# Kernel optimization log

Measured on AMD Instinct MI355X. Metric: run time of the kernel, lower is better.

## Reference

```python
import jax, jax.numpy as jnp
import numpy as np

RADIUS_IN, RADIUS_OUT, NSAMPLE = 0.4, 0.8, 32
SCENE = 10.0  # cube edge length for point coordinates


def setup_inputs() -> dict:
    key = jax.random.key(0)
    k1, k2, k3 = jax.random.split(key, 3)
    B, N, NP, C = 2, 16384, 4096, 64
    xyz = jax.random.uniform(k1, (B, N, 3), dtype=jnp.float32) * SCENE
    new_xyz = jax.random.uniform(k2, (B, NP, 3), dtype=jnp.float32) * SCENE
    features = jax.random.normal(k3, (B, C, N), dtype=jnp.float32)
    return {"xyz": xyz, "new_xyz": new_xyz, "features": features}


def ball_query_dilated(xyz, new_xyz, min_r, max_r, nsample):
    # xyz: (B,N,3), new_xyz: (B,P,3) -> idx: (B,P,nsample) int32
    N = xyz.shape[1]
    d2 = jnp.sum((new_xyz[:, :, None, :] - xyz[:, None, :, :]) ** 2, axis=-1)  # (B,P,N)
    mask = (d2 >= min_r * min_r) & (d2 < max_r * max_r)
    ar = jnp.arange(N, dtype=jnp.int32)
    # valid points keep their index; invalid pushed after all valid ones, in order
    sort_key = jnp.where(mask, ar, ar + N)
    _, idx_sorted = jax.lax.top_k(-sort_key, nsample)  # first nsample in-range point indices
    cnt = jnp.sum(mask, axis=-1)  # (B,P)
    slot_valid = jnp.arange(nsample, dtype=cnt.dtype)[None, None, :] < cnt[:, :, None]
    # CUDA kernel fills all slots with the first found index; if none found idx stays 0
    # (when cnt==0, idx_sorted[...,0] == 0 since key N is the minimum), so this matches.
    idx = jnp.where(slot_valid, idx_sorted, idx_sorted[:, :, :1])
    return idx.astype(jnp.int32)


def group(features, idx):
    # features: (B,C,N), idx: (B,P,S) -> (B,C,P,S)
    return jax.vmap(lambda f, i: f[:, i])(features, idx)


def reference(xyz, new_xyz, features):
    idx = ball_query_dilated(xyz, new_xyz, RADIUS_IN, RADIUS_OUT, NSAMPLE)
    xyz_t = jnp.transpose(xyz, (0, 2, 1))  # (B,3,N)
    grouped_xyz = group(xyz_t, idx) - jnp.transpose(new_xyz, (0, 2, 1))[:, :, :, None]
    grouped_features = group(features, idx)
    new_features = jnp.concatenate([grouped_xyz, grouped_features], axis=1)  # (B,3+C,P,S)
    return new_features
```

## Files before the change

### kernel.cpp

```cpp
#include <hip/hip_runtime.h>
#include <hip/hip_bf16.h>

#define BB 2
#define NN 16384
#define NP 4096
#define CC 64
#define SS 32
#define NCH (3 + CC)

#define NSUB 32
#define SUBN (NN / NSUB)

__global__ void __launch_bounds__(256) pack_xyz_kernel(
    const float* __restrict__ xyz, float4* __restrict__ xyz4)
{
    int i = blockIdx.x * 256 + threadIdx.x;
    if (i < BB * NN) {
        float4 v;
        v.x = xyz[3 * i + 0];
        v.y = xyz[3 * i + 1];
        v.z = xyz[3 * i + 2];
        v.w = 0.0f;
        xyz4[i] = v;
    }
}

__global__ void __launch_bounds__(256) transpose_feat_kernel(
    const float* __restrict__ f, float* __restrict__ ft)
{
    __shared__ float tile[64 * 65];
    const int b  = blockIdx.y;
    const int n0 = blockIdx.x * 64;
    const int t  = threadIdx.x;
    const int tn  = t & 63;
    const int tc4 = t >> 6;
#pragma unroll
    for (int r = 0; r < 16; ++r) {
        int c = r * 4 + tc4;
        tile[c * 65 + tn] = f[((b * CC + c) << 14) + n0 + tn];
    }
    __syncthreads();
#pragma unroll
    for (int r = 0; r < 16; ++r) {
        int nl = r * 4 + tc4;
        ft[((b << 14) + n0 + nl) * CC + tn] = tile[tn * 65 + nl];
    }
}

__global__ void __launch_bounds__(256) query_kernel(
    const float4* __restrict__ xyz4, const float* __restrict__ new_xyz,
    unsigned short* __restrict__ part, unsigned char* __restrict__ cntp)
{
#pragma clang fp contract(off)
    __shared__ float4 pts_s[SUBN];
    const int t   = threadIdx.x;
    const int sub = blockIdx.y;
    const int q   = blockIdx.x * 256 + t;
    const int b   = q >> 12;

    const float RMIN2 = (float)(0.4 * 0.4);
    const float RMAX2 = (float)(0.8 * 0.8);
    const unsigned ULO = __float_as_uint(RMIN2);
    const unsigned URNG = __float_as_uint(RMAX2) - ULO;

    const float4* __restrict__ pts = xyz4 + (b << 14) + sub * SUBN;
#pragma unroll
    for (int i = 0; i < SUBN / 256; ++i)
        pts_s[i * 256 + t] = pts[i * 256 + t];
    __syncthreads();

    const float qx = new_xyz[q * 3 + 0];
    const float qy = new_xyz[q * 3 + 1];
    const float qz = new_xyz[q * 3 + 2];

    unsigned short* __restrict__ mypart = part + (q * NSUB + sub) * SS;
    const int base = sub * SUBN;

    int cnt = 0;
    for (int j0 = 0; j0 < SUBN; j0 += 8) {
        float4 P[8];
#pragma unroll
        for (int k = 0; k < 8; ++k) P[k] = pts_s[j0 + k];
        unsigned m = 0;
#pragma unroll
        for (int k = 0; k < 8; ++k) {
            float dx = P[k].x - qx;
            float dy = P[k].y - qy;
            float dz = P[k].z - qz;
            float dx2 = dx * dx;
            float dy2 = dy * dy;
            float dz2 = dz * dz;
            float d2 = (dx2 + dy2) + dz2;
            unsigned ud = __float_as_uint(d2);
            bool valid = (ud - ULO) < URNG;
            m |= valid ? (1u << k) : 0u;
        }
        if (m) {
            do {
                int k = __ffs(m) - 1;
                m &= m - 1;
                if (cnt < SS) {
                    mypart[cnt] = (unsigned short)(base + j0 + k);
                    cnt++;
                }
            } while (m);
        }
    }
    cntp[q * NSUB + sub] = (unsigned char)cnt;
}

__global__ void __launch_bounds__(256) merge_kernel(
    const unsigned short* __restrict__ part, const unsigned char* __restrict__ cntp,
    int* __restrict__ idxg)
{
    const int lane = threadIdx.x & 63;
    const int w    = threadIdx.x >> 6;
    const int q    = blockIdx.x * 4 + w;

    int c = (lane < NSUB) ? (int)cntp[q * NSUB + lane] : 0;

    int off = c;
#pragma unroll
    for (int d = 1; d < 64; d <<= 1) {
        int v = __shfl_up(off, d);
        if (lane >= d) off += v;
    }
    int total = __shfl(off, 63);
    if (total > SS) total = SS;
    off -= c;

    const unsigned short* __restrict__ p = part + (q * NSUB + lane) * SS;
    int firstval = (c > 0) ? (int)p[0] : 0;
    unsigned long long m = __ballot(c > 0);
    int first = 0;
    if (m) {
        int fl = __ffsll((unsigned long long)m) - 1;
        first = __shfl(firstval, fl);
    }

    int* __restrict__ o = idxg + q * SS;
    for (int j = 0; j < c; ++j) {
        int s = off + j;
        if (s < SS) o[s] = (int)p[j];
    }
    if (lane < SS && lane >= total) o[lane] = first;
}

__global__ void __launch_bounds__(256) group_kernel(
    const float4* __restrict__ xyz4, const float* __restrict__ new_xyz,
    const float* __restrict__ ft, const int* __restrict__ idxg,
    float* __restrict__ out)
{
    __shared__ float tile[4][16 * 66];
    const int w    = threadIdx.x >> 6;
    const int lane = threadIdx.x & 63;
    const int q    = blockIdx.x * 4 + w;
    const int b    = q >> 12;
    const int p    = q & (NP - 1);
    const int s    = lane & 31;

    const int idxv = idxg[q * SS + s];

    float4 pt = xyz4[(b << 14) + idxv];
    float q0 = new_xyz[q * 3 + 0];
    float q1 = new_xyz[q * 3 + 1];
    float q2 = new_xyz[q * 3 + 2];
    if (lane < 32) {
        out[((b * NCH + 0) * NP + p) * SS + s] = pt.x - q0;
        out[((b * NCH + 1) * NP + p) * SS + s] = pt.y - q1;
        out[((b * NCH + 2) * NP + p) * SS + s] = pt.z - q2;
    }

    float* tl = tile[w];
    const float* __restrict__ ftb = ft + (b << 14) * CC;
    const int sl = lane & 15;
    const int cq = lane >> 4;
#pragma unroll
    for (int h = 0; h < 2; ++h) {
#pragma unroll
        for (int s2 = 0; s2 < 16; ++s2) {
            int n = __shfl(idxv, h * 16 + s2);
            tl[s2 * 66 + lane] = ftb[(n << 6) + lane];
        }
        asm volatile("s_waitcnt lgkmcnt(0)" ::: "memory");
#pragma unroll
        for (int cp = 0; cp < 16; ++cp) {
            int ch = cp * 4 + cq;
            out[((b * NCH + 3 + ch) * NP + p) * SS + h * 16 + sl] = tl[sl * 66 + ch];
        }
        asm volatile("s_waitcnt lgkmcnt(0)" ::: "memory");
    }
}

extern "C" void kernel_launch(void* const* d_in, const int* in_sizes, int n_in,
                              void* d_out, int out_size, void* d_ws, size_t ws_size,
                              hipStream_t stream)
{
    const float* xyz      = (const float*)d_in[0];
    const float* new_xyz  = (const float*)d_in[1];
    const float* features = (const float*)d_in[2];
    float* out = (float*)d_out;

    char* ws = (char*)d_ws;
    float4*         xyz4 = (float4*)(ws);
    float*          ft   = (float*)(ws + 524288);
    unsigned short* part = (unsigned short*)(ws + 8912896);
    unsigned char*  cntp = (unsigned char*)(ws + 25690112);
    int*            idxg = (int*)(ws + 25952256);

    hipLaunchKernelGGL(pack_xyz_kernel, dim3((BB * NN) / 256), dim3(256), 0, stream,
                       xyz, xyz4);
    hipLaunchKernelGGL(transpose_feat_kernel, dim3(NN / 64, BB), dim3(256), 0, stream,
                       features, ft);
    hipLaunchKernelGGL(query_kernel, dim3((BB * NP) / 256, NSUB), dim3(256), 0, stream,
                       xyz4, new_xyz, part, cntp);
    hipLaunchKernelGGL(merge_kernel, dim3((BB * NP) / 4), dim3(256), 0, stream,
                       part, cntp, idxg);
    hipLaunchKernelGGL(group_kernel, dim3((BB * NP) / 4), dim3(256), 0, stream,
                       xyz4, new_xyz, ft, idxg, out);
}
```

Before: 158.0 us.

## Parallelize ball query over points per wave with ballot-based compaction

Each wave now keeps 512 sub-block points in registers (8 per lane) and loops over 32 queries, which are broadcast through scalar loads. Matches are found with a wave ballot and written in order using popcount prefix offsets. This removes the per-thread serial scan of the sub-block, the shared-memory staging, and the divergent per-thread bit loop. In exchange it issues a ballot per point group and sends scattered 2-byte stores from many lanes to the same part row.

```diff
diff --git a/kernel.cpp b/kernel.cpp
--- a/kernel.cpp
+++ b/kernel.cpp
@@ -10,6 +10,7 @@
 
 #define NSUB 32
 #define SUBN (NN / NSUB)
+#define QB 32
 
 __global__ void __launch_bounds__(256) pack_xyz_kernel(
     const float* __restrict__ xyz, float4* __restrict__ xyz4)
@@ -52,36 +53,36 @@
     unsigned short* __restrict__ part, unsigned char* __restrict__ cntp)
 {
 #pragma clang fp contract(off)
-    __shared__ float4 pts_s[SUBN];
-    const int t   = threadIdx.x;
-    const int sub = blockIdx.y;
-    const int q   = blockIdx.x * 256 + t;
-    const int b   = q >> 12;
+    const int lane = threadIdx.x & 63;
+    const int wid  = blockIdx.x * 4 + (threadIdx.x >> 6);
+    const int b    = wid >> 12;
+    const int r    = wid & 4095;
+    const int sub  = r >> 7;
+    const int qb   = r & 127;
+    const int qbase = qb * QB;
 
     const float RMIN2 = (float)(0.4 * 0.4);
     const float RMAX2 = (float)(0.8 * 0.8);
-    const unsigned ULO = __float_as_uint(RMIN2);
+    const unsigned ULO  = __float_as_uint(RMIN2);
     const unsigned URNG = __float_as_uint(RMAX2) - ULO;
 
-    const float4* __restrict__ pts = xyz4 + (b << 14) + sub * SUBN;
-#pragma unroll
-    for (int i = 0; i < SUBN / 256; ++i)
-        pts_s[i * 256 + t] = pts[i * 256 + t];
-    __syncthreads();
-
-    const float qx = new_xyz[q * 3 + 0];
-    const float qy = new_xyz[q * 3 + 1];
-    const float qz = new_xyz[q * 3 + 2];
-
-    unsigned short* __restrict__ mypart = part + (q * NSUB + sub) * SS;
-    const int base = sub * SUBN;
-
-    int cnt = 0;
-    for (int j0 = 0; j0 < SUBN; j0 += 8) {
-        float4 P[8];
-#pragma unroll
-        for (int k = 0; k < 8; ++k) P[k] = pts_s[j0 + k];
-        unsigned m = 0;
+    const float4* __restrict__ pb = xyz4 + (b << 14) + sub * SUBN;
+    float4 P[8];
+#pragma unroll
+    for (int k = 0; k < 8; ++k) P[k] = pb[k * 64 + lane];
+
+    const unsigned long long ltmask = (1ull << lane) - 1ull;
+    int mycnt = 0;
+
+    for (int j = 0; j < QB; ++j) {
+        const int qg = b * NP + qbase + j;
+        const int qoff = __builtin_amdgcn_readfirstlane(qg * 3);
+        const float qx = new_xyz[qoff + 0];
+        const float qy = new_xyz[qoff + 1];
+        const float qz = new_xyz[qoff + 2];
+
+        unsigned short* __restrict__ mp = part + ((size_t)qg * NSUB + sub) * SS;
+        int cnt = 0;
 #pragma unroll
         for (int k = 0; k < 8; ++k) {
             float dx = P[k].x - qx;
@@ -91,22 +92,22 @@
             float dy2 = dy * dy;
             float dz2 = dz * dz;
             float d2 = (dx2 + dy2) + dz2;
-            unsigned ud = __float_as_uint(d2);
-            bool valid = (ud - ULO) < URNG;
-            m |= valid ? (1u << k) : 0u;
+            bool valid = (__float_as_uint(d2) - ULO) < URNG;
+            unsigned long long m = __ballot(valid);
+            if (m) {
+                if (valid) {
+                    int slot = cnt + (int)__popcll(m & ltmask);
+                    if (slot < SS)
+                        mp[slot] = (unsigned short)(sub * SUBN + k * 64 + lane);
+                }
+                cnt += (int)__popcll(m);
+            }
         }
-        if (m) {
-            do {
-                int k = __ffs(m) - 1;
-                m &= m - 1;
-                if (cnt < SS) {
-                    mypart[cnt] = (unsigned short)(base + j0 + k);
-                    cnt++;
-                }
-            } while (m);
-        }
-    }
-    cntp[q * NSUB + sub] = (unsigned char)cnt;
+        if (cnt > SS) cnt = SS;
+        mycnt = (lane == j) ? cnt : mycnt;
+    }
+    if (lane < QB)
+        cntp[(size_t)(b * NP + qbase + lane) * NSUB + sub] = (unsigned char)mycnt;
 }
 
 __global__ void __launch_bounds__(256) merge_kernel(
@@ -212,7 +213,7 @@
                        xyz, xyz4);
     hipLaunchKernelGGL(transpose_feat_kernel, dim3(NN / 64, BB), dim3(256), 0, stream,
                        features, ft);
-    hipLaunchKernelGGL(query_kernel, dim3((BB * NP) / 256, NSUB), dim3(256), 0, stream,
+    hipLaunchKernelGGL(query_kernel, dim3((BB * NSUB * (NP / QB)) / 4), dim3(256), 0, stream,
                        xyz4, new_xyz, part, cntp);
     hipLaunchKernelGGL(merge_kernel, dim3((BB * NP) / 4), dim3(256), 0, stream,
                        part, cntp, idxg);
```

New measurement: 146.1 us. 1.08x faster.
